# Kernel tuning notes

Hardware: AMD Instinct MI355X
Metric: run time of the kernel (lower is better)

Reference implementation:

```python
import jax, jax.numpy as jnp
import numpy as np

B, T, NLAT, N, D = 8, 4, 64, 2048, 1024
HEADS, HEAD_DIM = 16, 64
ADIM = HEADS * HEAD_DIM
EPS = 1e-5


def layer_norm(x, w, b):
    mu = jnp.mean(x, axis=-1, keepdims=True)
    var = jnp.var(x, axis=-1, keepdims=True)
    return (x - mu) * jax.lax.rsqrt(var + EPS) * w + b


def setup_inputs() -> dict:
    key = jax.random.key(0)
    ks = jax.random.split(key, 8)
    s = 0.02
    return {
        "latents": jax.random.normal(ks[0], (B, T, NLAT, D), jnp.float32),
        "x": jax.random.normal(ks[1], (B, T, N, D), jnp.float32),
        "Wq": jax.random.normal(ks[2], (D, ADIM), jnp.float32) * s,     # [in, out]
        "Wkv": jax.random.normal(ks[3], (D, 2 * ADIM), jnp.float32) * s,
        "Wout": jax.random.normal(ks[4], (ADIM, D), jnp.float32) * s,
        "bout": jnp.zeros((D,), jnp.float32),
        "lnl_w": jnp.ones((D,), jnp.float32),
        "lnl_b": jnp.zeros((D,), jnp.float32),
        "lnm_w": jnp.ones((D,), jnp.float32),
        "lnm_b": jnp.zeros((D,), jnp.float32),
    }


def reference(latents, x, Wq, Wkv, Wout, bout, lnl_w, lnl_b, lnm_w, lnm_b):
    scale = HEAD_DIM ** (-0.5)
    lat = layer_norm(latents, lnl_w, lnl_b)          # [B,T,NLAT,D]
    med = layer_norm(x, lnm_w, lnm_b)                # [B,T,N,D]
    q = lat @ Wq                                      # [B,T,NLAT,ADIM]
    kv_in = jnp.concatenate((med, lat), axis=-2)      # [B,T,N+NLAT,D]
    kv = kv_in @ Wkv                                  # [B,T,N+NLAT,2*ADIM]
    k, v = jnp.split(kv, 2, axis=-1)
    # split heads: b t n (h d) -> b h t n d
    def split_heads(z):
        b, t, n, _ = z.shape
        return z.reshape(b, t, n, HEADS, HEAD_DIM).transpose(0, 3, 1, 2, 4)
    q = split_heads(q) * scale
    k = split_heads(k)
    v = split_heads(v)
    scores = jnp.einsum('bhtid,bhtjd->bhtij', q, k)   # [B,H,T,NLAT,N+NLAT]
    attn = jax.nn.softmax(scores, axis=-1)            # max-subtract handled internally
    out = jnp.einsum('bhtij,bhtjd->bhtid', attn, v)   # [B,H,T,NLAT,HEAD_DIM]
    out = out.transpose(0, 2, 3, 1, 4).reshape(B, T, NLAT, ADIM)
    return out @ Wout + bout
```

## Files before the change

### kernel.cpp

```cpp
#include <hip/hip_runtime.h>
#include <hip/hip_bf16.h>
#include <stdint.h>

#define B_    8
#define T_    4
#define NLAT  64
#define NMED  2048
#define NKV   2112
#define D_    1024
#define HEADS 16
#define HD    64
#define ADIM  1024
#define BT    32

#define GK    1024
#define GN    2048
#define GM    67584
#define MT2   264
#define NSLC  32

typedef __attribute__((ext_vector_type(8))) short bf16x8;
typedef __attribute__((ext_vector_type(4))) float f32x4;

__device__ __forceinline__ ushort f2bf(float f) {
  union { float f; uint32_t u; } v; v.f = f;
  return (ushort)((v.u + 0x7fff + ((v.u >> 16) & 1)) >> 16);
}

__device__ __forceinline__ void gload_lds16(const void* g, void* l) {
  __builtin_amdgcn_global_load_lds(
      (const __attribute__((address_space(1))) void*)g,
      (__attribute__((address_space(3))) void*)l, 16, 0, 0);
}

__device__ __forceinline__ f32x4 mfma16(bf16x8 a, bf16x8 b, f32x4 c) {
  return __builtin_amdgcn_mfma_f32_16x16x32_bf16(a, b, c, 0, 0, 0);
}

__global__ __launch_bounds__(256) void wtrans(const float* __restrict__ src,
                                              ushort* __restrict__ dst,
                                              int K, int Nm) {
  __shared__ float t[64][65];
  const int tr = blockIdx.y, tc = blockIdx.x;
  const int c = threadIdx.x & 63;
  const int r4 = threadIdx.x >> 6;
#pragma unroll
  for (int rr = 0; rr < 16; ++rr) {
    int r = r4 + rr * 4;
    t[r][c] = src[(size_t)(tr * 64 + r) * Nm + tc * 64 + c];
  }
  __syncthreads();
#pragma unroll
  for (int rr = 0; rr < 16; ++rr) {
    int n = r4 + rr * 4;
    dst[(size_t)(tc * 64 + n) * K + tr * 64 + c] = f2bf(t[c][n]);
  }
}

__global__ __launch_bounds__(256) void ln_kernel(
    const float* __restrict__ lat, const float* __restrict__ x,
    const float* __restrict__ lnl_w, const float* __restrict__ lnl_b,
    const float* __restrict__ lnm_w, const float* __restrict__ lnm_b,
    ushort* __restrict__ kvin) {
  const int row = blockIdx.x;
  const int bt = row / NKV;
  const int j = row - bt * NKV;
  const float* src;
  const float* w;
  const float* bb;
  if (j < NMED) {
    src = x + ((size_t)bt * NMED + j) * D_;
    w = lnm_w; bb = lnm_b;
  } else {
    src = lat + ((size_t)bt * NLAT + (j - NMED)) * D_;
    w = lnl_w; bb = lnl_b;
  }
  const int tid = threadIdx.x;
  float4 v = ((const float4*)src)[tid];
  float s = v.x + v.y + v.z + v.w;
  float s2 = v.x * v.x + v.y * v.y + v.z * v.z + v.w * v.w;
#pragma unroll
  for (int off = 1; off < 64; off <<= 1) {
    s += __shfl_xor(s, off, 64);
    s2 += __shfl_xor(s2, off, 64);
  }
  __shared__ float red[8];
  const int wave = tid >> 6;
  if ((tid & 63) == 0) { red[wave] = s; red[4 + wave] = s2; }
  __syncthreads();
  float S = red[0] + red[1] + red[2] + red[3];
  float S2 = red[4] + red[5] + red[6] + red[7];
  const float inv = 1.f / (float)D_;
  float mu = S * inv;
  float var = S2 * inv - mu * mu;
  float rs = rsqrtf(var + 1e-5f);
  float4 wv = ((const float4*)w)[tid];
  float4 bv = ((const float4*)bb)[tid];
  ushort4 ov;
  ov.x = f2bf((v.x - mu) * rs * wv.x + bv.x);
  ov.y = f2bf((v.y - mu) * rs * wv.y + bv.y);
  ov.z = f2bf((v.z - mu) * rs * wv.z + bv.z);
  ov.w = f2bf((v.w - mu) * rs * wv.w + bv.w);
  ((ushort4*)(kvin + (size_t)row * D_))[tid] = ov;
}

template <int AMODE, int OUTMODE>
__global__ __launch_bounds__(256) void gemm_bt(const ushort* __restrict__ A,
                                               const ushort* __restrict__ Bt,
                                               void* __restrict__ C,
                                               const float* __restrict__ bias,
                                               int M, int N, int K, int ldc) {
  __shared__ ushort lsA[128 * 32];
  __shared__ ushort lsB[128 * 32];
  const int tid = threadIdx.x;
  const int lane = tid & 63;
  const int wave = tid >> 6;
  const int brow = blockIdx.y * 128;
  const int bcol = blockIdx.x * 128;
  const int wr = (wave >> 1) * 64;
  const int wc = (wave & 1) * 64;
  const int lr = lane & 15;
  const int lk = (lane >> 4) * 8;

  f32x4 acc[4][4];
#pragma unroll
  for (int m = 0; m < 4; ++m)
#pragma unroll
    for (int n = 0; n < 4; ++n) acc[m][n] = (f32x4){0.f, 0.f, 0.f, 0.f};

  const int wbase = (tid & 192) * 16;

  for (int k0 = 0; k0 < K; k0 += 32) {
#pragma unroll
    for (int i = 0; i < 2; ++i) {
      int idx = i * 256 + tid;
      int r = idx >> 2;
      int cc = (idx & 3) * 8;
      long arow;
      if (AMODE == 1) {
        int gr = brow + r;
        arow = (long)(gr >> 6) * NKV + NMED + (gr & 63);
      } else {
        arow = brow + r;
      }
      gload_lds16(A + arow * (long)K + k0 + cc, (char*)lsA + i * 4096 + wbase);
      gload_lds16(Bt + (long)(bcol + r) * K + k0 + cc, (char*)lsB + i * 4096 + wbase);
    }
    __syncthreads();

    bf16x8 af[4], bf[4];
#pragma unroll
    for (int m = 0; m < 4; ++m)
      af[m] = *(const bf16x8*)&lsA[(wr + m * 16 + lr) * 32 + lk];
#pragma unroll
    for (int n = 0; n < 4; ++n)
      bf[n] = *(const bf16x8*)&lsB[(wc + n * 16 + lr) * 32 + lk];
#pragma unroll
    for (int m = 0; m < 4; ++m)
#pragma unroll
      for (int n = 0; n < 4; ++n) acc[m][n] = mfma16(af[m], bf[n], acc[m][n]);
    __syncthreads();
  }

#pragma unroll
  for (int m = 0; m < 4; ++m) {
#pragma unroll
    for (int n = 0; n < 4; ++n) {
      int row0 = brow + wr + m * 16 + (lane >> 4) * 4;
      int col = bcol + wc + n * 16 + lr;
#pragma unroll
      for (int r = 0; r < 4; ++r) {
        long off = (long)(row0 + r) * ldc + col;
        float v = acc[m][n][r];
        if (OUTMODE == 1) ((ushort*)C)[off] = f2bf(v * 0.125f);
        else ((float*)C)[off] = v + bias[col];
      }
    }
  }
}

__global__ __launch_bounds__(512, 2) void gemm256(const ushort* __restrict__ A,
                                                  const ushort* __restrict__ Bt,
                                                  ushort* __restrict__ C) {
  extern __shared__ __align__(16) char smem[];
  const int tid = threadIdx.x;
  const int lane = tid & 63;
  const int wv = tid >> 6;
  const int wm = wv >> 2;
  const int wn = wv & 3;
  const int lr = lane & 15;
  const int lg = lane >> 4;

  const int g = blockIdx.x;
  const int v = (g & 7) * MT2 + (g >> 3);
  const int bx = v & 7;
  const int by = v >> 3;
  const long brow = (long)by * 256;
  const int bcol = bx * 256;

  const int pcx = lg ^ ((lr >> 1) & 3);
  const int rbA = wm * 128 + lr;
  const int rbB = wn * 64 + lr;

  f32x4 acc[8][4];
#pragma unroll
  for (int m = 0; m < 8; ++m)
#pragma unroll
    for (int n = 0; n < 4; ++n) acc[m][n] = (f32x4){0.f, 0.f, 0.f, 0.f};

  const int s0 = tid, s1 = 512 + tid;
  const int r0 = s0 >> 2, r1 = s1 >> 2;
  const int c0 = (s0 & 3) ^ ((s0 >> 3) & 3);
  const int c1 = (s1 & 3) ^ ((s1 >> 3) & 3);
  const int o0 = (s0 & ~63) * 16;
  const int o1 = (s1 & ~63) * 16;

#define STAGE_A(slc, slot)                                                     \
  {                                                                            \
    long k0 = (long)(slc) * 32;                                                \
    char* db = smem + (slot) * 32768;                                          \
    gload_lds16(A + (brow + r0) * (long)GK + k0 + c0 * 8, db + o0);            \
    gload_lds16(A + (brow + r1) * (long)GK + k0 + c1 * 8, db + o1);            \
  }
#define STAGE_B(slc, slot)                                                     \
  {                                                                            \
    long k0 = (long)(slc) * 32;                                                \
    char* db = smem + (slot) * 32768 + 16384;                                  \
    gload_lds16(Bt + (long)(bcol + r0) * GK + k0 + c0 * 8, db + o0);           \
    gload_lds16(Bt + (long)(bcol + r1) * GK + k0 + c1 * 8, db + o1);           \
  }

  bf16x8 a0[4], a1[4], b0[4], b1[4];

  STAGE_A(0, 0); STAGE_B(0, 0);
  STAGE_A(1, 1); STAGE_B(1, 1);
  STAGE_A(2, 2); STAGE_B(2, 2);
  asm volatile("s_waitcnt vmcnt(8)" ::: "memory");
  __builtin_amdgcn_s_barrier();
#pragma unroll
  for (int m = 0; m < 4; ++m)
    a0[m] = *(const bf16x8*)(smem + (rbA + m * 16) * 64 + pcx * 16);
#pragma unroll
  for (int n = 0; n < 4; ++n)
    b0[n] = *(const bf16x8*)(smem + 16384 + (rbB + n * 16) * 64 + pcx * 16);
  __builtin_amdgcn_sched_barrier(0);

#define SLICE(T, BCUR, BNXT)                                                   \
  {                                                                            \
    const int t_ = (T);                                                        \
    const char* sA_ = smem + (t_ & 3) * 32768;                                 \
    const int ts_ = (t_ + 3 < NSLC) ? t_ + 3 : t_;                             \
    const int ws_ = (t_ + 3) & 3;                                              \
                                                        \
    _Pragma("unroll")                                                          \
    for (int m = 0; m < 4; ++m)                                                \
      a1[m] = *(const bf16x8*)(sA_ + (rbA + (m + 4) * 16) * 64 + pcx * 16);    \
    STAGE_A(ts_, ws_);                                                         \
    __builtin_amdgcn_sched_barrier(0);                                         \
    __builtin_amdgcn_s_barrier();                                              \
    asm volatile("s_waitcnt lgkmcnt(4)" ::: "memory");                         \
    __builtin_amdgcn_sched_barrier(0);                                         \
    __builtin_amdgcn_s_setprio(1);                                             \
    _Pragma("unroll")                                                          \
    for (int m = 0; m < 4; ++m)                                                \
      _Pragma("unroll")                                                        \
      for (int n = 0; n < 4; ++n)                                              \
        acc[m][n] = mfma16(BCUR[n], a0[m], acc[m][n]);                         \
    __builtin_amdgcn_s_setprio(0);                                             \
    __builtin_amdgcn_sched_barrier(0);                                         \
    __builtin_amdgcn_s_barrier();                                              \
                                                        \
    STAGE_B(ts_, ws_);                                                         \
    asm volatile("s_waitcnt vmcnt(8)" ::: "memory");                           \
    __builtin_amdgcn_sched_barrier(0);                                         \
    __builtin_amdgcn_s_barrier();                                              \
    {                                                                          \
      const int tn_ = (t_ + 1 < NSLC) ? t_ + 1 : t_;                           \
      const char* nA_ = smem + (tn_ & 3) * 32768;                              \
      const char* nB_ = nA_ + 16384;                                           \
      _Pragma("unroll")                                                        \
      for (int m = 0; m < 4; ++m)                                              \
        a0[m] = *(const bf16x8*)(nA_ + (rbA + m * 16) * 64 + pcx * 16);        \
      _Pragma("unroll")                                                        \
      for (int n = 0; n < 4; ++n)                                              \
        BNXT[n] = *(const bf16x8*)(nB_ + (rbB + n * 16) * 64 + pcx * 16);      \
    }                                                                          \
    __builtin_amdgcn_sched_barrier(0);                                         \
    asm volatile("s_waitcnt lgkmcnt(8)" ::: "memory");                         \
    __builtin_amdgcn_sched_barrier(0);                                         \
    __builtin_amdgcn_s_setprio(1);                                             \
    _Pragma("unroll")                                                          \
    for (int m = 0; m < 4; ++m)                                                \
      _Pragma("unroll")                                                        \
      for (int n = 0; n < 4; ++n)                                              \
        acc[m + 4][n] = mfma16(BCUR[n], a1[m], acc[m + 4][n]);                 \
    __builtin_amdgcn_s_setprio(0);                                             \
    __builtin_amdgcn_sched_barrier(0);                                         \
    __builtin_amdgcn_s_barrier();                                              \
  }

  for (int t = 0; t < NSLC; t += 2) {
    SLICE(t, b0, b1);
    SLICE(t + 1, b1, b0);
  }
#undef SLICE
#undef STAGE_A
#undef STAGE_B

#pragma unroll
  for (int m = 0; m < 8; ++m) {
    long row = brow + wm * 128 + m * 16 + lr;
    ushort* crow = C + row * GN + bcol + wn * 64 + lg * 4;
#pragma unroll
    for (int n = 0; n < 4; ++n) {
      ushort4 o;
      o.x = f2bf(acc[m][n][0]);
      o.y = f2bf(acc[m][n][1]);
      o.z = f2bf(acc[m][n][2]);
      o.w = f2bf(acc[m][n][3]);
      *(ushort4*)(crow + n * 16) = o;
    }
  }
}

__global__ __launch_bounds__(256) void attn_kernel(const ushort* __restrict__ q,
                                                   const ushort* __restrict__ kv,
                                                   ushort* __restrict__ o) {
  const int blk = blockIdx.x;
  const int bt = blk >> 4;
  const int h = blk & 15;
  const int tid = threadIdx.x;
  const int wave = tid >> 6;
  const int lane = tid & 63;
  const int lr = lane & 15;
  const int lg = lane >> 4;

  __shared__ ushort vt[64][72];
  __shared__ ushort pl[4][16][72];

  const ushort* qbase = q + (size_t)(bt * 64 + wave * 16) * ADIM + h * HD;
  bf16x8 qf[2];
#pragma unroll
  for (int ks = 0; ks < 2; ++ks)
    qf[ks] = *(const bf16x8*)(qbase + (size_t)lr * ADIM + ks * 32 + lg * 8);

  const ushort* kvb = kv + (size_t)bt * NKV * 2048;

  f32x4 accO[4];
#pragma unroll
  for (int n = 0; n < 4; ++n) accO[n] = (f32x4){0.f, 0.f, 0.f, 0.f};
  float mrun[4] = {-1e30f, -1e30f, -1e30f, -1e30f};
  float lrun[4] = {0.f, 0.f, 0.f, 0.f};

  for (int jt = 0; jt < NKV / 64; ++jt) {
    const int j0 = jt * 64;
    __syncthreads();

    {
      int jj = tid >> 2;
      int dbase = (tid & 3) * 16;
#pragma unroll
      for (int half = 0; half < 2; ++half) {
        int d0 = dbase + half * 8;
        bf16x8 vv = *(const bf16x8*)(kvb + (size_t)(j0 + jj) * 2048 + ADIM + h * HD + d0);
#pragma unroll
        for (int e = 0; e < 8; ++e) vt[d0 + e][jj] = ((const ushort*)&vv)[e];
      }
    }

    f32x4 s[4];
#pragma unroll
    for (int nj = 0; nj < 4; ++nj) s[nj] = (f32x4){0.f, 0.f, 0.f, 0.f};
#pragma unroll
    for (int nj = 0; nj < 4; ++nj)
#pragma unroll
      for (int ks = 0; ks < 2; ++ks) {
        bf16x8 kf = *(const bf16x8*)(kvb + (size_t)(j0 + nj * 16 + lr) * 2048 +
                                     h * HD + ks * 32 + lg * 8);
        s[nj] = mfma16(qf[ks], kf, s[nj]);
      }

    float mt[4], corr[4], psum[4];
#pragma unroll
    for (int r = 0; r < 4; ++r)
      mt[r] = fmaxf(fmaxf(s[0][r], s[1][r]), fmaxf(s[2][r], s[3][r]));
#pragma unroll
    for (int off = 1; off < 16; off <<= 1)
#pragma unroll
      for (int r = 0; r < 4; ++r) mt[r] = fmaxf(mt[r], __shfl_xor(mt[r], off, 64));
#pragma unroll
    for (int r = 0; r < 4; ++r) {
      float mn = fmaxf(mrun[r], mt[r]);
      corr[r] = __expf(mrun[r] - mn);
      mrun[r] = mn;
      psum[r] = 0.f;
    }
#pragma unroll
    for (int nj = 0; nj < 4; ++nj)
#pragma unroll
      for (int r = 0; r < 4; ++r) {
        float pv = __expf(s[nj][r] - mrun[r]);
        s[nj][r] = pv;
        psum[r] += pv;
      }
#pragma unroll
    for (int off = 1; off < 16; off <<= 1)
#pragma unroll
      for (int r = 0; r < 4; ++r) psum[r] += __shfl_xor(psum[r], off, 64);
#pragma unroll
    for (int r = 0; r < 4; ++r) lrun[r] = lrun[r] * corr[r] + psum[r];
#pragma unroll
    for (int n = 0; n < 4; ++n)
#pragma unroll
      for (int r = 0; r < 4; ++r) accO[n][r] *= corr[r];

#pragma unroll
    for (int nj = 0; nj < 4; ++nj)
#pragma unroll
      for (int r = 0; r < 4; ++r)
        pl[wave][lg * 4 + r][nj * 16 + lr] = f2bf(s[nj][r]);
    __syncthreads();

    bf16x8 pf[2];
#pragma unroll
    for (int ks = 0; ks < 2; ++ks)
      pf[ks] = *(const bf16x8*)&pl[wave][lr][ks * 32 + lg * 8];
#pragma unroll
    for (int nd = 0; nd < 4; ++nd)
#pragma unroll
      for (int ks = 0; ks < 2; ++ks) {
        bf16x8 vf = *(const bf16x8*)&vt[nd * 16 + lr][ks * 32 + lg * 8];
        accO[nd] = mfma16(pf[ks], vf, accO[nd]);
      }
  }

#pragma unroll
  for (int nd = 0; nd < 4; ++nd)
#pragma unroll
    for (int r = 0; r < 4; ++r) {
      float vv = accO[nd][r] / lrun[r];
      int row = bt * 64 + wave * 16 + lg * 4 + r;
      o[(size_t)row * ADIM + h * HD + nd * 16 + lr] = f2bf(vv);
    }
}

extern "C" void kernel_launch(void* const* d_in, const int* in_sizes, int n_in,
                              void* d_out, int out_size, void* d_ws, size_t ws_size,
                              hipStream_t stream) {
  const float* latents = (const float*)d_in[0];
  const float* x = (const float*)d_in[1];
  const float* Wq = (const float*)d_in[2];
  const float* Wkv = (const float*)d_in[3];
  const float* Wout = (const float*)d_in[4];
  const float* bout = (const float*)d_in[5];
  const float* lnl_w = (const float*)d_in[6];
  const float* lnl_b = (const float*)d_in[7];
  const float* lnm_w = (const float*)d_in[8];
  const float* lnm_b = (const float*)d_in[9];

  char* ws = (char*)d_ws;
  size_t off = 0;
  auto alloc = [&](size_t bytes) -> void* {
    void* p = ws + off;
    off += (bytes + 255) & ~(size_t)255;
    return p;
  };
  ushort* kvin = (ushort*)alloc((size_t)BT * NKV * D_ * 2);
  ushort* kvo  = (ushort*)alloc((size_t)BT * NKV * 2048 * 2);
  ushort* qb   = (ushort*)alloc((size_t)BT * NLAT * ADIM * 2);
  ushort* ao   = (ushort*)alloc((size_t)BT * NLAT * ADIM * 2);
  ushort* WqT  = (ushort*)alloc((size_t)D_ * ADIM * 2);
  ushort* WkvT = (ushort*)alloc((size_t)D_ * 2 * ADIM * 2);
  ushort* WoutT = (ushort*)alloc((size_t)ADIM * D_ * 2);

  hipFuncSetAttribute((const void*)gemm256,
                      hipFuncAttributeMaxDynamicSharedMemorySize, 131072);

  wtrans<<<dim3(ADIM / 64, D_ / 64), 256, 0, stream>>>(Wq, WqT, D_, ADIM);
  wtrans<<<dim3(2 * ADIM / 64, D_ / 64), 256, 0, stream>>>(Wkv, WkvT, D_, 2 * ADIM);
  wtrans<<<dim3(D_ / 64, ADIM / 64), 256, 0, stream>>>(Wout, WoutT, ADIM, D_);

  ln_kernel<<<BT * NKV, 256, 0, stream>>>(latents, x, lnl_w, lnl_b, lnm_w, lnm_b, kvin);

  gemm_bt<1, 1><<<dim3(ADIM / 128, BT * NLAT / 128), 256, 0, stream>>>(
      kvin, WqT, qb, nullptr, BT * NLAT, ADIM, D_, ADIM);

  gemm256<<<dim3(MT2 * 8), 512, 131072, stream>>>(kvin, WkvT, kvo);

  attn_kernel<<<BT * HEADS, 256, 0, stream>>>(qb, kvo, ao);

  gemm_bt<0, 2><<<dim3(D_ / 128, BT * NLAT / 128), 256, 0, stream>>>(
      ao, WoutT, d_out, bout, BT * NLAT, D_, ADIM, D_);
}
```

Before: 596.6 us.

## Stage K in swizzled LDS with register prefetch; swizzle small GEMM tiles

The attention kernel now loads each K/V tile into registers one iteration ahead and stores K into an XOR-swizzled LDS buffer, instead of having every wave read K straight from global memory. This is meant to hide global latency and stop the waves from fetching the same K data repeatedly. The small Q and output GEMMs get an XCD-aware block remap, XOR-swizzled LDS layout, swapped MFMA operands for vectorized 4-wide stores, and a 3-blocks-per-CU launch bound. The cost is extra LDS use, an added barrier per tile, and more register pressure from the prefetch.

```diff
diff --git a/kernel.cpp b/kernel.cpp
--- a/kernel.cpp
+++ b/kernel.cpp
@@ -105,22 +105,30 @@
 }
 
 template <int AMODE, int OUTMODE>
-__global__ __launch_bounds__(256) void gemm_bt(const ushort* __restrict__ A,
-                                               const ushort* __restrict__ Bt,
-                                               void* __restrict__ C,
-                                               const float* __restrict__ bias,
-                                               int M, int N, int K, int ldc) {
+__global__ __launch_bounds__(256, 3) void gemm128(const ushort* __restrict__ A,
+                                                  const ushort* __restrict__ Bt,
+                                                  void* __restrict__ C,
+                                                  const float* __restrict__ bias,
+                                                  int ntx, int nwg, int K, int ldc) {
   __shared__ ushort lsA[128 * 32];
   __shared__ ushort lsB[128 * 32];
   const int tid = threadIdx.x;
   const int lane = tid & 63;
   const int wave = tid >> 6;
-  const int brow = blockIdx.y * 128;
-  const int bcol = blockIdx.x * 128;
+  const int lr = lane & 15;
+  const int lg = lane >> 4;
   const int wr = (wave >> 1) * 64;
   const int wc = (wave & 1) * 64;
-  const int lr = lane & 15;
-  const int lk = (lane >> 4) * 8;
+
+  const int g = blockIdx.x;
+  const int cpx = nwg >> 3;
+  const int v = (g & 7) * cpx + (g >> 3);
+  const int bx = v % ntx;
+  const int by = v / ntx;
+  const long brow = (long)by * 128;
+  const int bcol = bx * 128;
+
+  const int pcx = lg ^ ((lr >> 1) & 3);
 
   f32x4 acc[4][4];
 #pragma unroll
@@ -128,52 +136,70 @@
 #pragma unroll
     for (int n = 0; n < 4; ++n) acc[m][n] = (f32x4){0.f, 0.f, 0.f, 0.f};
 
-  const int wbase = (tid & 192) * 16;
+  const int s0 = tid, s1 = 256 + tid;
+  const int r0 = s0 >> 2, r1 = s1 >> 2;
+  const int c0 = (s0 & 3) ^ ((s0 >> 3) & 3);
+  const int c1 = (s1 & 3) ^ ((s1 >> 3) & 3);
+  const int o0 = (s0 & ~63) * 16;
+  const int o1 = (s1 & ~63) * 16;
+
+  long arow0, arow1;
+  if (AMODE == 1) {
+    int g0 = (int)brow + r0, g1 = (int)brow + r1;
+    arow0 = (long)(g0 >> 6) * NKV + NMED + (g0 & 63);
+    arow1 = (long)(g1 >> 6) * NKV + NMED + (g1 & 63);
+  } else {
+    arow0 = brow + r0;
+    arow1 = brow + r1;
+  }
+  const long browB0 = (long)(bcol + r0) * K;
+  const long browB1 = (long)(bcol + r1) * K;
 
   for (int k0 = 0; k0 < K; k0 += 32) {
-#pragma unroll
-    for (int i = 0; i < 2; ++i) {
-      int idx = i * 256 + tid;
-      int r = idx >> 2;
-      int cc = (idx & 3) * 8;
-      long arow;
-      if (AMODE == 1) {
-        int gr = brow + r;
-        arow = (long)(gr >> 6) * NKV + NMED + (gr & 63);
+    gload_lds16(A + arow0 * (long)K + k0 + c0 * 8, (char*)lsA + o0);
+    gload_lds16(A + arow1 * (long)K + k0 + c1 * 8, (char*)lsA + o1);
+    gload_lds16(Bt + browB0 + k0 + c0 * 8, (char*)lsB + o0);
+    gload_lds16(Bt + browB1 + k0 + c1 * 8, (char*)lsB + o1);
+    __syncthreads();
+
+    bf16x8 af[4], bf[4];
+#pragma unroll
+    for (int m = 0; m < 4; ++m)
+      af[m] = *(const bf16x8*)((char*)lsA + (wr + m * 16 + lr) * 64 + pcx * 16);
+#pragma unroll
+    for (int n = 0; n < 4; ++n)
+      bf[n] = *(const bf16x8*)((char*)lsB + (wc + n * 16 + lr) * 64 + pcx * 16);
+#pragma unroll
+    for (int m = 0; m < 4; ++m)
+#pragma unroll
+      for (int n = 0; n < 4; ++n)
+        acc[m][n] = mfma16(bf[n], af[m], acc[m][n]);
+    __syncthreads();
+  }
+
+#pragma unroll
+  for (int m = 0; m < 4; ++m) {
+    long row = brow + wr + m * 16 + lr;
+#pragma unroll
+    for (int n = 0; n < 4; ++n) {
+      int coln = bcol + wc + n * 16 + lg * 4;
+      long off = row * (long)ldc + coln;
+      if (OUTMODE == 2) {
+        float4 bv = *(const float4*)(bias + coln);
+        float4 o;
+        o.x = acc[m][n][0] + bv.x;
+        o.y = acc[m][n][1] + bv.y;
+        o.z = acc[m][n][2] + bv.z;
+        o.w = acc[m][n][3] + bv.w;
+        *(float4*)((float*)C + off) = o;
       } else {
-        arow = brow + r;
-      }
-      gload_lds16(A + arow * (long)K + k0 + cc, (char*)lsA + i * 4096 + wbase);
-      gload_lds16(Bt + (long)(bcol + r) * K + k0 + cc, (char*)lsB + i * 4096 + wbase);
-    }
-    __syncthreads();
-
-    bf16x8 af[4], bf[4];
-#pragma unroll
-    for (int m = 0; m < 4; ++m)
-      af[m] = *(const bf16x8*)&lsA[(wr + m * 16 + lr) * 32 + lk];
-#pragma unroll
-    for (int n = 0; n < 4; ++n)
-      bf[n] = *(const bf16x8*)&lsB[(wc + n * 16 + lr) * 32 + lk];
-#pragma unroll
-    for (int m = 0; m < 4; ++m)
-#pragma unroll
-      for (int n = 0; n < 4; ++n) acc[m][n] = mfma16(af[m], bf[n], acc[m][n]);
-    __syncthreads();
-  }
-
-#pragma unroll
-  for (int m = 0; m < 4; ++m) {
-#pragma unroll
-    for (int n = 0; n < 4; ++n) {
-      int row0 = brow + wr + m * 16 + (lane >> 4) * 4;
-      int col = bcol + wc + n * 16 + lr;
-#pragma unroll
-      for (int r = 0; r < 4; ++r) {
-        long off = (long)(row0 + r) * ldc + col;
-        float v = acc[m][n][r];
-        if (OUTMODE == 1) ((ushort*)C)[off] = f2bf(v * 0.125f);
-        else ((float*)C)[off] = v + bias[col];
+        const float sc = (OUTMODE == 1) ? 0.125f : 1.f;
+        ushort4 o;
+        o.x = f2bf(acc[m][n][0] * sc);
+        o.y = f2bf(acc[m][n][1] * sc);
+        o.z = f2bf(acc[m][n][2] * sc);
+        o.w = f2bf(acc[m][n][3] * sc);
+        *(ushort4*)((ushort*)C + off) = o;
       }
     }
   }
@@ -337,6 +363,7 @@
 
   __shared__ ushort vt[64][72];
   __shared__ ushort pl[4][16][72];
+  __shared__ ushort kl[64 * 64];
 
   const ushort* qbase = q + (size_t)(bt * 64 + wave * 16) * ADIM + h * HD;
   bf16x8 qf[2];
@@ -345,6 +372,8 @@
     qf[ks] = *(const bf16x8*)(qbase + (size_t)lr * ADIM + ks * 32 + lg * 8);
 
   const ushort* kvb = kv + (size_t)bt * NKV * 2048;
+  const int jj = tid >> 2;
+  const int q4 = tid & 3;
 
   f32x4 accO[4];
 #pragma unroll
@@ -352,22 +381,42 @@
   float mrun[4] = {-1e30f, -1e30f, -1e30f, -1e30f};
   float lrun[4] = {0.f, 0.f, 0.f, 0.f};
 
+  bf16x8 kr0, kr1, vr0, vr1;
+  {
+    const ushort* src = kvb + (size_t)jj * 2048 + h * HD + q4 * 16;
+    kr0 = *(const bf16x8*)(src);
+    kr1 = *(const bf16x8*)(src + 8);
+    vr0 = *(const bf16x8*)(src + ADIM);
+    vr1 = *(const bf16x8*)(src + ADIM + 8);
+  }
+
   for (int jt = 0; jt < NKV / 64; ++jt) {
-    const int j0 = jt * 64;
     __syncthreads();
 
     {
-      int jj = tid >> 2;
-      int dbase = (tid & 3) * 16;
-#pragma unroll
-      for (int half = 0; half < 2; ++half) {
-        int d0 = dbase + half * 8;
-        bf16x8 vv = *(const bf16x8*)(kvb + (size_t)(j0 + jj) * 2048 + ADIM + h * HD + d0);
-#pragma unroll
-        for (int e = 0; e < 8; ++e) vt[d0 + e][jj] = ((const ushort*)&vv)[e];
+      int p0 = (q4 * 2) ^ (jj & 7);
+      int p1 = (q4 * 2 + 1) ^ (jj & 7);
+      *(bf16x8*)((char*)kl + jj * 128 + p0 * 16) = kr0;
+      *(bf16x8*)((char*)kl + jj * 128 + p1 * 16) = kr1;
+      int d0 = q4 * 16;
+#pragma unroll
+      for (int e = 0; e < 8; ++e) {
+        vt[d0 + e][jj] = ((const ushort*)&vr0)[e];
+        vt[d0 + 8 + e][jj] = ((const ushort*)&vr1)[e];
       }
     }
 
+    bf16x8 nk0, nk1, nv0, nv1;
+    {
+      const int tn = (jt + 1 < NKV / 64) ? jt + 1 : jt;
+      const ushort* src = kvb + (size_t)(tn * 64 + jj) * 2048 + h * HD + q4 * 16;
+      nk0 = *(const bf16x8*)(src);
+      nk1 = *(const bf16x8*)(src + 8);
+      nv0 = *(const bf16x8*)(src + ADIM);
+      nv1 = *(const bf16x8*)(src + ADIM + 8);
+    }
+    __syncthreads();
+
     f32x4 s[4];
 #pragma unroll
     for (int nj = 0; nj < 4; ++nj) s[nj] = (f32x4){0.f, 0.f, 0.f, 0.f};
@@ -375,8 +424,9 @@
     for (int nj = 0; nj < 4; ++nj)
 #pragma unroll
       for (int ks = 0; ks < 2; ++ks) {
-        bf16x8 kf = *(const bf16x8*)(kvb + (size_t)(j0 + nj * 16 + lr) * 2048 +
-                                     h * HD + ks * 32 + lg * 8);
+        int row = nj * 16 + lr;
+        int phys = (4 * ks + lg) ^ (lr & 7);
+        bf16x8 kf = *(const bf16x8*)((char*)kl + row * 128 + phys * 16);
         s[nj] = mfma16(qf[ks], kf, s[nj]);
       }
 
@@ -432,6 +482,8 @@
         bf16x8 vf = *(const bf16x8*)&vt[nd * 16 + lr][ks * 32 + lg * 8];
         accO[nd] = mfma16(pf[ks], vf, accO[nd]);
       }
+
+    kr0 = nk0; kr1 = nk1; vr0 = nv0; vr1 = nv1;
   }
 
 #pragma unroll
@@ -482,13 +534,13 @@
 
   ln_kernel<<<BT * NKV, 256, 0, stream>>>(latents, x, lnl_w, lnl_b, lnm_w, lnm_b, kvin);
 
-  gemm_bt<1, 1><<<dim3(ADIM / 128, BT * NLAT / 128), 256, 0, stream>>>(
-      kvin, WqT, qb, nullptr, BT * NLAT, ADIM, D_, ADIM);
+  gemm128<1, 1><<<dim3(128), 256, 0, stream>>>(
+      kvin, WqT, qb, nullptr, ADIM / 128, 128, D_, ADIM);
 
   gemm256<<<dim3(MT2 * 8), 512, 131072, stream>>>(kvin, WkvT, kvo);
 
   attn_kernel<<<BT * HEADS, 256, 0, stream>>>(qb, kvo, ao);
 
-  gemm_bt<0, 2><<<dim3(D_ / 128, BT * NLAT / 128), 256, 0, stream>>>(
-      ao, WoutT, d_out, bout, BT * NLAT, D_, ADIM, D_);
-}
+  gemm128<0, 2><<<dim3(128), 256, 0, stream>>>(
+      ao, WoutT, d_out, bout, D_ / 128, 128, ADIM, D_);
+}
```

Result: faster. 555.5 us (-6.9%).
